# Kernel optimization log

Hardware: AMD Instinct MI355X
Metric: run time of the kernel (lower is better)

The kernel has to match this reference:

```python
import jax, jax.numpy as jnp
from jax import lax
import numpy as np

VOCAB = 100000
MAX_SEQ = 8192
DIM = 128
K = 5
STRIDE = 1
PAD = 2


def setup_inputs() -> dict:
    key = jax.random.key(0)
    ks = jax.random.split(key, 6)
    X = jax.random.randint(ks[0], (8, 8192), 0, VOCAB, dtype=jnp.int64)
    # nn.Linear(vocab, dim): weight (dim, vocab), bias (dim)
    W_lin = jax.random.normal(ks[1], (DIM, VOCAB), dtype=jnp.float32) * 0.02
    b_lin = jax.random.normal(ks[2], (DIM,), dtype=jnp.float32) * 0.02
    # nn.Conv1d(dim, dim, k): weight (out=dim, in=dim, k), bias (dim)
    W_conv = jax.random.normal(ks[3], (DIM, DIM, K), dtype=jnp.float32) * 0.02
    b_conv = jax.random.normal(ks[4], (DIM,), dtype=jnp.float32) * 0.02
    # nn.Embedding(max_seq_len, dim)
    pos_table = jax.random.normal(ks[5], (MAX_SEQ, DIM), dtype=jnp.float32) * 0.02
    return {"X": X, "W_lin": W_lin, "b_lin": b_lin,
            "W_conv": W_conv, "b_conv": b_conv, "pos_table": pos_table}


def reference(X, W_lin, b_lin, W_conv, b_conv, pos_table):
    # one_hot(X) @ W_lin.T + b_lin  ==  gather rows of W_lin.T
    emb = jnp.take(W_lin.T, X, axis=0) + b_lin          # (b, n, d)
    x = jnp.transpose(emb, (0, 2, 1))                   # (b, d, n)
    y = lax.conv_general_dilated(
        x, W_conv, window_strides=(STRIDE,), padding=[(PAD, PAD)],
        dimension_numbers=("NCH", "OIH", "NCH"))
    y = y + b_conv[None, :, None]                       # (b, d, n_out)
    tokens = jnp.transpose(y, (0, 2, 1))                # (b, n_out, d)
    n_out = tokens.shape[1]
    return tokens + pos_table[:n_out][None, :, :]
```

## Files before the change

### kernel.cpp

```cpp
#include <hip/hip_runtime.h>
#include <hip/hip_bf16.h>
#include <stdint.h>

#define VOCAB 100000
#define SEQ   8192
#define BATCH 8
#define DIM   128

#define WLT_BLOCKS 1563
#define WCONV_BLOCKS 320

typedef short bf16x8 __attribute__((ext_vector_type(8)));
typedef float f32x4  __attribute__((ext_vector_type(4)));

__device__ __forceinline__ ushort f2bf(float f) {
  union { float f; uint32_t u; } v; v.f = f;
  uint32_t u = v.u;
  return (ushort)((u + 0x7FFF + ((u >> 16) & 1)) >> 16);
}

__global__ __launch_bounds__(256) void prep(
    const float* __restrict__ wlin, const float* __restrict__ blin,
    const float* __restrict__ wconv, ushort* __restrict__ wlt,
    ushort* __restrict__ wcb) {
  __shared__ float tile[128 * 65];
  const int tid = threadIdx.x;

  if (blockIdx.x >= WLT_BLOCKS) {
    int e = (blockIdx.x - WLT_BLOCKS) * 256 + tid;
    int k = e / (DIM * DIM);
    int rem = e % (DIM * DIM);
    int d = rem / DIM, i = rem % DIM;
    wcb[e] = f2bf(wconv[(d * DIM + i) * 5 + k]);
    return;
  }

  const int t0 = blockIdx.x * 64;

  const int c4 = (tid & 15) * 4;
  const int rbase = tid >> 4;
  const bool cvalid = (t0 + c4) < VOCAB;
#pragma unroll
  for (int p = 0; p < 8; ++p) {
    int r = p * 16 + rbase;
    float4 v = make_float4(0.f, 0.f, 0.f, 0.f);
    if (cvalid) v = *(const float4*)(wlin + (size_t)r * VOCAB + t0 + c4);
    float* dst = &tile[r * 65 + c4];
    dst[0] = v.x; dst[1] = v.y; dst[2] = v.z; dst[3] = v.w;
  }
  __syncthreads();

  const int chunk = tid & 15;
  float bias8[8];
#pragma unroll
  for (int j = 0; j < 8; ++j) bias8[j] = blin[chunk * 8 + j];

#pragma unroll
  for (int p = 0; p < 4; ++p) {
    int tl = (tid >> 4) + p * 16;
    int t  = t0 + tl;
    if (t >= VOCAB) continue;
    ushort u[8];
#pragma unroll
    for (int j = 0; j < 8; ++j)
      u[j] = f2bf(tile[(chunk * 8 + j) * 65 + tl] + bias8[j]);
    *(uint4*)(wlt + (size_t)t * DIM + chunk * 8) = *(const uint4*)u;
  }
}

template <bool EDGE>
__device__ __forceinline__ void conv_wave(
    const int* __restrict__ Xb, const ushort* __restrict__ wlt,
    const ushort* __restrict__ Blds, const float* __restrict__ bconv,
    const float* __restrict__ pos, float* __restrict__ outb,
    int n0, int q, int lane, int lr, int lq) {
  int  tok[2][5];
  bool vld[2][5];
#pragma unroll
  for (int mt = 0; mt < 2; ++mt)
#pragma unroll
    for (int k = 0; k < 5; ++k) {
      int n = n0 + mt * 16 + lr + k - 2;
      bool v = EDGE ? (n >= 0 && n < SEQ) : true;
      vld[mt][k] = v;
      tok[mt][k] = v ? Xb[n] : 0;
    }

  f32x4 acc[2][2];
#pragma unroll
  for (int a = 0; a < 2; ++a)
#pragma unroll
    for (int b = 0; b < 2; ++b) acc[a][b] = (f32x4)0.f;

  const int colA = lq * 8;
#pragma unroll
  for (int k = 0; k < 5; ++k) {
    bf16x8 A[2][4];
#pragma unroll
    for (int mt = 0; mt < 2; ++mt)
#pragma unroll
      for (int kk = 0; kk < 4; ++kk) {
        bf16x8 v = *(const bf16x8*)(wlt + ((size_t)tok[mt][k] << 7) + kk * 32 + colA);
        A[mt][kk] = (EDGE && !vld[mt][k]) ? (bf16x8)(short)0 : v;
      }
#pragma unroll
    for (int kk = 0; kk < 4; ++kk) {
      bf16x8 B[2];
#pragma unroll
      for (int nt = 0; nt < 2; ++nt)
        B[nt] = *(const bf16x8*)(Blds + (((k * 4 + kk) * 2 + nt) << 9) + lane * 8);
#pragma unroll
      for (int mt = 0; mt < 2; ++mt)
#pragma unroll
        for (int nt = 0; nt < 2; ++nt)
          acc[mt][nt] = __builtin_amdgcn_mfma_f32_16x16x32_bf16(
              A[mt][kk], B[nt], acc[mt][nt], 0, 0, 0);
    }
  }

  float bc[2];
#pragma unroll
  for (int nt = 0; nt < 2; ++nt) bc[nt] = bconv[q * 32 + nt * 16 + lr];
#pragma unroll
  for (int mt = 0; mt < 2; ++mt) {
#pragma unroll
    for (int rr = 0; rr < 4; ++rr) {
      int gn = n0 + mt * 16 + lq * 4 + rr;
      const float* posrow = pos + (size_t)gn * DIM;
      float* orow = outb + (size_t)gn * DIM;
#pragma unroll
      for (int nt = 0; nt < 2; ++nt) {
        int d = q * 32 + nt * 16 + lr;
        orow[d] = acc[mt][nt][rr] + bc[nt] + posrow[d];
      }
    }
  }
}

__global__ __launch_bounds__(256, 4) void conv_main(
    const int* __restrict__ X, const ushort* __restrict__ wlt,
    const ushort* __restrict__ wcb, const float* __restrict__ bconv,
    const float* __restrict__ pos, float* __restrict__ out) {
  __shared__ __align__(16) ushort Blds[20480];

  const int tid = threadIdx.x;
  const int q   = blockIdx.x & 3;
  const int gb  = blockIdx.x >> 2;
  const int batch = gb >> 6;
  const int nbb   = (gb & 63) << 7;

#pragma unroll
  for (int it = 0; it < 10; ++it) {
    int s  = it * 256 + tid;
    int f  = s >> 6, l = s & 63;
    int k  = f >> 3, kk = (f >> 1) & 3, nt = f & 1;
    int flr = l & 15, flq = l >> 4;
    int d  = q * 32 + nt * 16 + flr;
    uint4 v = *(const uint4*)(wcb + ((size_t)(k * DIM + d) * DIM + kk * 32 + flq * 8));
    *(uint4*)&Blds[s * 8] = v;
  }
  __syncthreads();

  const int wave = tid >> 6;
  const int lane = tid & 63;
  const int lr   = lane & 15;
  const int lq   = lane >> 4;
  const int n0   = nbb + wave * 32;
  const int* Xb  = X + batch * SEQ;
  float* outb    = out + (size_t)batch * SEQ * DIM;

  if (n0 == 0 || n0 == SEQ - 32)
    conv_wave<true>(Xb, wlt, Blds, bconv, pos, outb, n0, q, lane, lr, lq);
  else
    conv_wave<false>(Xb, wlt, Blds, bconv, pos, outb, n0, q, lane, lr, lq);
}

extern "C" void kernel_launch(void* const* d_in, const int* in_sizes, int n_in,
                              void* d_out, int out_size, void* d_ws, size_t ws_size,
                              hipStream_t stream) {
  const int*   X     = (const int*)d_in[0];
  const float* wlin  = (const float*)d_in[1];
  const float* blin  = (const float*)d_in[2];
  const float* wconv = (const float*)d_in[3];
  const float* bconv = (const float*)d_in[4];
  const float* pos   = (const float*)d_in[5];
  float*       out   = (float*)d_out;

  ushort* wcb = (ushort*)d_ws;
  ushort* wlt = (ushort*)((char*)d_ws + 262144);

  hipLaunchKernelGGL(prep, dim3(WLT_BLOCKS + WCONV_BLOCKS), dim3(256), 0, stream,
                     wlin, blin, wconv, wlt, wcb);
  hipLaunchKernelGGL(conv_main, dim3(2048), dim3(256), 0, stream,
                     X, wlt, wcb, bconv, pos, out);
}
```

Baseline: 160.5 us.

## Prefetch next tap's gathered rows, use nontemporal prep stores, reorder block mapping

The conv loop now double-buffers the gathered embedding rows, issuing loads for tap k+1 before the MFMAs of tap k so gather latency overlaps compute. The prep kernel writes its bf16 tables with nontemporal stores. Block indexing changes so consecutive blocks share the same output-column quarter q instead of the same token range, which changes L2 locality for the weight tables and the gathered rows. Double-buffering raises register pressure under the 4-blocks-per-SM launch bound, and the remapping may hurt reuse of gathered rows across the four q blocks.

```diff
diff --git a/kernel.cpp b/kernel.cpp
--- a/kernel.cpp
+++ b/kernel.cpp
@@ -12,6 +12,7 @@
 
 typedef short bf16x8 __attribute__((ext_vector_type(8)));
 typedef float f32x4  __attribute__((ext_vector_type(4)));
+typedef uint  u32x4  __attribute__((ext_vector_type(4)));
 
 __device__ __forceinline__ ushort f2bf(float f) {
   union { float f; uint32_t u; } v; v.f = f;
@@ -31,7 +32,7 @@
     int k = e / (DIM * DIM);
     int rem = e % (DIM * DIM);
     int d = rem / DIM, i = rem % DIM;
-    wcb[e] = f2bf(wconv[(d * DIM + i) * 5 + k]);
+    __builtin_nontemporal_store(f2bf(wconv[(d * DIM + i) * 5 + k]), &wcb[e]);
     return;
   }
 
@@ -64,7 +65,8 @@
 #pragma unroll
     for (int j = 0; j < 8; ++j)
       u[j] = f2bf(tile[(chunk * 8 + j) * 65 + tl] + bias8[j]);
-    *(uint4*)(wlt + (size_t)t * DIM + chunk * 8) = *(const uint4*)u;
+    __builtin_nontemporal_store(*(const u32x4*)u,
+                                (u32x4*)(wlt + (size_t)t * DIM + chunk * 8));
   }
 }
 
@@ -93,16 +95,28 @@
     for (int b = 0; b < 2; ++b) acc[a][b] = (f32x4)0.f;
 
   const int colA = lq * 8;
+
+  bf16x8 A[2][4];
+#pragma unroll
+  for (int mt = 0; mt < 2; ++mt)
+#pragma unroll
+    for (int kk = 0; kk < 4; ++kk) {
+      bf16x8 v = *(const bf16x8*)(wlt + ((size_t)tok[mt][0] << 7) + kk * 32 + colA);
+      A[mt][kk] = (EDGE && !vld[mt][0]) ? (bf16x8)(short)0 : v;
+    }
+
 #pragma unroll
   for (int k = 0; k < 5; ++k) {
-    bf16x8 A[2][4];
-#pragma unroll
-    for (int mt = 0; mt < 2; ++mt)
-#pragma unroll
-      for (int kk = 0; kk < 4; ++kk) {
-        bf16x8 v = *(const bf16x8*)(wlt + ((size_t)tok[mt][k] << 7) + kk * 32 + colA);
-        A[mt][kk] = (EDGE && !vld[mt][k]) ? (bf16x8)(short)0 : v;
-      }
+    bf16x8 An[2][4];
+    if (k < 4) {
+#pragma unroll
+      for (int mt = 0; mt < 2; ++mt)
+#pragma unroll
+        for (int kk = 0; kk < 4; ++kk) {
+          bf16x8 v = *(const bf16x8*)(wlt + ((size_t)tok[mt][k + 1] << 7) + kk * 32 + colA);
+          An[mt][kk] = (EDGE && !vld[mt][k + 1]) ? (bf16x8)(short)0 : v;
+        }
+    }
 #pragma unroll
     for (int kk = 0; kk < 4; ++kk) {
       bf16x8 B[2];
@@ -115,6 +129,12 @@
         for (int nt = 0; nt < 2; ++nt)
           acc[mt][nt] = __builtin_amdgcn_mfma_f32_16x16x32_bf16(
               A[mt][kk], B[nt], acc[mt][nt], 0, 0, 0);
+    }
+    if (k < 4) {
+#pragma unroll
+      for (int mt = 0; mt < 2; ++mt)
+#pragma unroll
+        for (int kk = 0; kk < 4; ++kk) A[mt][kk] = An[mt][kk];
     }
   }
 
@@ -144,8 +164,8 @@
   __shared__ __align__(16) ushort Blds[20480];
 
   const int tid = threadIdx.x;
-  const int q   = blockIdx.x & 3;
-  const int gb  = blockIdx.x >> 2;
+  const int q   = blockIdx.x >> 9;
+  const int gb  = blockIdx.x & 511;
   const int batch = gb >> 6;
   const int nbb   = (gb & 63) << 7;
 
```

Result: no change. 161.7 us (+0.8%).
